# Performance work log

Hardware: AMD Instinct MI355X
Metric: run time of the kernel (lower is better)

The kernel has to match this reference:

```python
import jax, jax.numpy as jnp
import numpy as np

VOXEL_LENGTH = 1.2


def grid_sample_3d_border(vol, grid):
    """torch.nn.functional.grid_sample (5D, bilinear, align_corners=False,
    padding_mode='border') with grid flattened to (B, N, 3) in (x, y, z) order.
    vol: (B, C, D, H, W). Returns (B, C, N)."""

    def sample_one(v, g):
        C, D, H, W = v.shape
        x, y, z = g[:, 0], g[:, 1], g[:, 2]
        # align_corners=False unnormalization
        ix = ((x + 1.0) * W - 1.0) * 0.5
        iy = ((y + 1.0) * H - 1.0) * 0.5
        iz = ((z + 1.0) * D - 1.0) * 0.5
        ix0f, iy0f, iz0f = jnp.floor(ix), jnp.floor(iy), jnp.floor(iz)
        wx, wy, wz = ix - ix0f, iy - iy0f, iz - iz0f
        # border padding: clamp indices, keep unclamped weights
        x0 = jnp.clip(ix0f, 0, W - 1).astype(jnp.int32)
        x1 = jnp.clip(ix0f + 1, 0, W - 1).astype(jnp.int32)
        y0 = jnp.clip(iy0f, 0, H - 1).astype(jnp.int32)
        y1 = jnp.clip(iy0f + 1, 0, H - 1).astype(jnp.int32)
        z0 = jnp.clip(iz0f, 0, D - 1).astype(jnp.int32)
        z1 = jnp.clip(iz0f + 1, 0, D - 1).astype(jnp.int32)
        vflat = v.reshape(C, D * H * W)

        def gather(zi, yi, xi):  # -> (C, N)
            return vflat[:, (zi * H + yi) * W + xi]

        out = (
            gather(z0, y0, x0) * ((1 - wz) * (1 - wy) * (1 - wx))
            + gather(z0, y0, x1) * ((1 - wz) * (1 - wy) * wx)
            + gather(z0, y1, x0) * ((1 - wz) * wy * (1 - wx))
            + gather(z0, y1, x1) * ((1 - wz) * wy * wx)
            + gather(z1, y0, x0) * (wz * (1 - wy) * (1 - wx))
            + gather(z1, y0, x1) * (wz * (1 - wy) * wx)
            + gather(z1, y1, x0) * (wz * wy * (1 - wx))
            + gather(z1, y1, x1) * (wz * wy * wx)
        )
        return out

    return jax.vmap(sample_one)(vol, grid)


def setup_inputs() -> dict:
    key = jax.random.key(0)
    ks = jax.random.split(key, 16)
    B, IMG, STEPS = 2, 64, 24
    N = IMG * IMG * STEPS
    C_IN, HID, RES = 32, 256, 32
    # points in world space, inside the voxel cube [-0.6, 0.6]
    points = jax.random.uniform(ks[0], (B, N, 3), jnp.float32) * 1.2 - 0.6
    feature_volume = jax.random.normal(ks[1], (B, C_IN, RES, RES, RES), jnp.float32)

    def lin(k, fan_in, fan_out, scale):
        kw, kb = jax.random.split(k)
        W = jax.random.uniform(kw, (fan_out, fan_in), jnp.float32, -scale, scale)
        b = jax.random.uniform(kb, (fan_out,), jnp.float32, -scale, scale)
        return W, b

    freq = 12.0
    W0, b0 = lin(ks[2], C_IN, HID, 1.0 / C_IN)  # first_layer_film_sine_init
    W1, b1 = lin(ks[3], HID, HID, float(np.sqrt(6.0 / HID) / freq))
    W2, b2 = lin(ks[4], HID, HID, float(np.sqrt(6.0 / HID) / freq))
    W3, b3 = lin(ks[5], HID, HID, float(np.sqrt(6.0 / HID) / freq))
    Wf, bf = lin(ks[6], HID, 4, float(np.sqrt(6.0 / HID) / freq))
    return {
        "points": points, "feature_volume": feature_volume,
        "W0": W0, "b0": b0, "W1": W1, "b1": b1, "W2": W2, "b2": b2,
        "W3": W3, "b3": b3, "Wf": Wf, "bf": bf,
        "img_size": 64, "num_steps": 24,
    }


def reference(points, feature_volume, W0, b0, W1, b1, W2, b2, W3, b3, Wf, bf,
              img_size, num_steps):
    grid = points / (VOXEL_LENGTH / 2.0)  # (B, N, 3) in [-1, 1]
    feats = grid_sample_3d_border(feature_volume, grid)  # (B, C, N)
    x = feats.transpose(0, 2, 1)  # (B, N, C)
    for W, b in ((W0, b0), (W1, b1), (W2, b2), (W3, b3)):
        x = jnp.sin(jnp.einsum('bnc,hc->bnh', x, W) + b)
    rgb_sigma = jnp.einsum('bnh,oh->bno', x, Wf) + bf  # (B, N, 4)
    rgb = jax.nn.sigmoid(rgb_sigma[..., :3])
    sigma = rgb_sigma[..., 3:4]
    return jnp.concatenate([rgb, sigma], axis=-1)
```

## Files before the change

### kernel.cpp

```cpp
#include <hip/hip_runtime.h>
#include <math.h>

#define THREADS 256

typedef __attribute__((ext_vector_type(8))) short bf16x8;
typedef __attribute__((ext_vector_type(4))) float f32x4;

#define INV2PI 0.15915494309189535f

#define NCHUNK 26
#define STREAM_BYTES (NCHUNK * 16384)
#define SBIAS_BYTES 4096

__device__ __host__ __forceinline__ int sigma_k(int k) {
    return (k & 0xE1) | ((k & 0x04) << 2) | ((k & 0x18) >> 1) | (k & 0x02);
}

__device__ __forceinline__ ushort f2bf(float f) {
    union { float f; unsigned u; } v; v.f = f;
    unsigned r = v.u + 0x7FFFu + ((v.u >> 16) & 1u);
    return (ushort)(r >> 16);
}

__device__ __forceinline__ float fast_sigmoid(float x) {
    return 1.0f / (1.0f + __expf(-x));
}

__device__ __forceinline__ unsigned cvt_pk_bf16(float lo, float hi) {
    unsigned d;
    asm("v_cvt_pk_bf16_f32 %0, %1, %2" : "=v"(d) : "v"(lo), "v"(hi));
    return d;
}

__device__ __forceinline__ float hw_sin(float x) {
    float r;
    asm("v_sin_f32 %0, %1" : "=v"(r) : "v"(x));
    return r;
}

__global__ void build_frags(const float* __restrict__ W0,
                            const float* __restrict__ W1,
                            const float* __restrict__ W2,
                            const float* __restrict__ W3,
                            const float* __restrict__ Wf,
                            ushort* __restrict__ stream) {
    const int gid = blockIdx.x * 256 + threadIdx.x;
    const int f = gid >> 6;
    if (f >= 416) return;
    const int lane = gid & 63;
    const int p16 = lane & 15, g = lane >> 4;
    ushort* dst = stream + (size_t)f * 512 + lane * 8;

    if (f < 16) {
        const float* row = W0 + (size_t)(f * 16 + p16) * 32;
#pragma unroll
        for (int i = 0; i < 8; ++i) dst[i] = f2bf(row[8 * g + i] * INV2PI);
    } else if (f < 400) {
        const int t = f - 16;
        const int h = t >> 7;
        const int r = t & 127;
        const int sub = r >> 4;
        const int idx = r & 15;
        const int q = sub & 1;
        const int kq = sub >> 1;
        const int ksl = idx >> 3;
        const int ntl = idx & 7;
        const int nt = q * 8 + ntl;
        const int ks = kq * 2 + ksl;
        const float* W = (h == 0) ? W1 : (h == 1) ? W2 : W3;
        const float* row = W + (size_t)(nt * 16 + p16) * 256;
#pragma unroll
        for (int i = 0; i < 8; ++i) dst[i] = f2bf(row[sigma_k(32 * ks + 8 * g + i)] * INV2PI);
    } else if (f < 408) {
        const int ks = f - 400;
        if (p16 < 4) {
            const float* row = Wf + (size_t)p16 * 256;
#pragma unroll
            for (int i = 0; i < 8; ++i) dst[i] = f2bf(row[sigma_k(32 * ks + 8 * g + i)]);
        } else {
#pragma unroll
            for (int i = 0; i < 8; ++i) dst[i] = 0;
        }
    } else {
#pragma unroll
        for (int i = 0; i < 8; ++i) dst[i] = 0;
    }
}

__global__ void scale_biases(const float* __restrict__ b0, const float* __restrict__ b1,
                             const float* __restrict__ b2, const float* __restrict__ b3,
                             float* __restrict__ sb) {
    const int i = blockIdx.x * 256 + threadIdx.x;
    const int l = i >> 8, j = i & 255;
    const float* b = (l == 0) ? b0 : (l == 1) ? b1 : (l == 2) ? b2 : b3;
    sb[i] = b[j] * INV2PI;
}

__global__ void vol_chlast(const float* __restrict__ vol, float* __restrict__ dst, int nvox) {
    int v = blockIdx.x * 256 + threadIdx.x;
    if (v >= nvox) return;
    const int b = v >> 15, idx = v & 32767;
    const float* s = vol + (size_t)b * 32 * 32768 + idx;
    float* d = dst + (size_t)v * 32;
#pragma unroll
    for (int c = 0; c < 32; ++c) d[c] = s[(size_t)c * 32768];
}

#define MF(a, b, c) __builtin_amdgcn_mfma_f32_16x16x32_bf16((a), (b), (c), 0, 0, 0)

__global__ __launch_bounds__(THREADS, 2)
void siren_pl(const float* __restrict__ points,
              const float* __restrict__ vol,
              const float* __restrict__ bfin,
              const ushort* __restrict__ Wstream,
              const float* __restrict__ sb,
              const float* __restrict__ volcl, int use_cl,
              float* __restrict__ out, long long total, int N) {
    __shared__ ushort ring[3 * 8192];

    const int tid = (int)threadIdx.x;
    const int w = tid >> 6;
    const int lane = tid & 63;
    const int p16 = lane & 15;
    const int g = lane >> 4;

    const long long base = (long long)blockIdx.x * 128;

    auto stage = [&](int c) {
        if (c >= NCHUNK) return;
        const ushort* src = Wstream + (size_t)c * 8192;
        ushort* dstbase = ring + (c % 3) * 8192;
#pragma unroll
        for (int q = 0; q < 4; ++q) {
            const int off = (q * 4 + w) * 512;
            __builtin_amdgcn_global_load_lds(
                (const __attribute__((address_space(1))) unsigned int*)(src + off + lane * 8),
                (__attribute__((address_space(3))) unsigned int*)(dstbase + off),
                16, 0, 0);
        }
    };
    stage(0);
    stage(1);
    stage(2);

    bf16x8 af0[2];
    {
#pragma unroll
        for (int ptt = 0; ptt < 2; ++ptt) {
            const long long gidx = base + w * 32 + ptt * 16 + p16;
            const long long gp = gidx < total ? gidx : total - 1;
            const int bi = (int)(gp / N);
            const float* pp = points + gp * 3;
            const float sc = 1.0f / 0.6f;
            const float ix = (pp[0] * sc + 1.0f) * 16.0f - 0.5f;
            const float iy = (pp[1] * sc + 1.0f) * 16.0f - 0.5f;
            const float iz = (pp[2] * sc + 1.0f) * 16.0f - 0.5f;
            const float fx = floorf(ix), fy = floorf(iy), fz = floorf(iz);
            const float wx = ix - fx, wy = iy - fy, wz = iz - fz;
            const int x0 = (int)fminf(fmaxf(fx, 0.0f), 31.0f);
            const int x1 = (int)fminf(fmaxf(fx + 1.0f, 0.0f), 31.0f);
            const int y0 = (int)fminf(fmaxf(fy, 0.0f), 31.0f);
            const int y1 = (int)fminf(fmaxf(fy + 1.0f, 0.0f), 31.0f);
            const int z0 = (int)fminf(fmaxf(fz, 0.0f), 31.0f);
            const int z1 = (int)fminf(fmaxf(fz + 1.0f, 0.0f), 31.0f);
            const int i000 = (z0 * 32 + y0) * 32 + x0, i001 = (z0 * 32 + y0) * 32 + x1;
            const int i010 = (z0 * 32 + y1) * 32 + x0, i011 = (z0 * 32 + y1) * 32 + x1;
            const int i100 = (z1 * 32 + y0) * 32 + x0, i101 = (z1 * 32 + y0) * 32 + x1;
            const int i110 = (z1 * 32 + y1) * 32 + x0, i111 = (z1 * 32 + y1) * 32 + x1;
            const float omx = 1.0f - wx, omy = 1.0f - wy, omz = 1.0f - wz;
            const float w000 = omz * omy * omx, w001 = omz * omy * wx;
            const float w010 = omz * wy * omx,  w011 = omz * wy * wx;
            const float w100 = wz * omy * omx,  w101 = wz * omy * wx;
            const float w110 = wz * wy * omx,   w111 = wz * wy * wx;

            f32x4 a[2];
            if (use_cl) {
                const float* vb = volcl + (size_t)bi * 32768 * 32 + g * 8;
#pragma unroll
                for (int h = 0; h < 2; ++h) {
                    const float* vh = vb + h * 4;
                    a[h]  = w000 * *(const f32x4*)(vh + (size_t)i000 * 32);
                    a[h] += w001 * *(const f32x4*)(vh + (size_t)i001 * 32);
                    a[h] += w010 * *(const f32x4*)(vh + (size_t)i010 * 32);
                    a[h] += w011 * *(const f32x4*)(vh + (size_t)i011 * 32);
                    a[h] += w100 * *(const f32x4*)(vh + (size_t)i100 * 32);
                    a[h] += w101 * *(const f32x4*)(vh + (size_t)i101 * 32);
                    a[h] += w110 * *(const f32x4*)(vh + (size_t)i110 * 32);
                    a[h] += w111 * *(const f32x4*)(vh + (size_t)i111 * 32);
                }
            } else {
                const float* vb = vol + ((size_t)bi * 32 + (size_t)g * 8) * 32768;
#pragma unroll
                for (int c = 0; c < 8; ++c) {
                    const float* vc = vb + (size_t)c * 32768;
                    a[c >> 2][c & 3] =
                        vc[i000] * w000 + vc[i001] * w001 + vc[i010] * w010 + vc[i011] * w011 +
                        vc[i100] * w100 + vc[i101] * w101 + vc[i110] * w110 + vc[i111] * w111;
                }
            }
            union { bf16x8 v; unsigned u[4]; } pk;
            pk.u[0] = cvt_pk_bf16(a[0][0], a[0][1]);
            pk.u[1] = cvt_pk_bf16(a[0][2], a[0][3]);
            pk.u[2] = cvt_pk_bf16(a[1][0], a[1][1]);
            pk.u[3] = cvt_pk_bf16(a[1][2], a[1][3]);
            af0[ptt] = pk.v;
        }
    }

    f32x4 accA[2][8];
    f32x4 accB[2][8];
    bf16x8 bfr[2][8];
    bf16x8 wreg[8];

    auto frag_at = [&](int slot, int idx) -> bf16x8 {
        return *(const bf16x8*)&ring[slot * 8192 + idx * 512 + lane * 8];
    };
    auto init_half = [&](f32x4 (&A)[2][8], const float* __restrict__ b, int ntbase) {
#pragma unroll
        for (int m = 0; m < 8; ++m) {
            const f32x4 bv = *(const f32x4*)&b[(ntbase + m) * 16 + 4 * g];
            A[0][m] = bv; A[1][m] = bv;
        }
    };
    auto pack_half = [&](f32x4 (&A)[2][8], int ksbase) {
#pragma unroll
        for (int ptt = 0; ptt < 2; ++ptt)
#pragma unroll
            for (int ks2 = 0; ks2 < 4; ++ks2) {
                union { bf16x8 v; unsigned u[4]; } pk;
#pragma unroll
                for (int j = 0; j < 4; ++j) {
                    const int m = 2 * ks2 + (j >> 1);
                    const int r = 2 * (j & 1);
                    pk.u[j] = cvt_pk_bf16(hw_sin(A[ptt][m][r]), hw_sin(A[ptt][m][r + 1]));
                }
                bfr[ptt][ksbase + ks2] = pk.v;
            }
    };
    auto mfma_half = [&](int kq, int ksl, f32x4 (&A)[2][8], int nslot, int nbase) {
        const bf16x8 bA = bfr[0][kq * 2 + ksl];
        const bf16x8 bB = bfr[1][kq * 2 + ksl];
        __builtin_amdgcn_s_setprio(1);
#pragma unroll
        for (int ntl = 0; ntl < 8; ++ntl) {
            A[0][ntl] = MF(wreg[ntl], bA, A[0][ntl]);
            A[1][ntl] = MF(wreg[ntl], bB, A[1][ntl]);
            wreg[ntl] = frag_at(nslot, nbase + ntl);
        }
        __builtin_amdgcn_s_setprio(0);
    };

    init_half(accA, sb, 0);
    init_half(accB, sb, 8);
    __syncthreads();

#pragma unroll
    for (int i = 0; i < 8; ++i) wreg[i] = frag_at(0, i);

    __builtin_amdgcn_s_setprio(1);
#pragma unroll
    for (int ntl = 0; ntl < 8; ++ntl) {
        accA[0][ntl] = MF(wreg[ntl], af0[0], accA[0][ntl]);
        accA[1][ntl] = MF(wreg[ntl], af0[1], accA[1][ntl]);
        wreg[ntl] = frag_at(0, 8 + ntl);
    }
#pragma unroll
    for (int ntl = 0; ntl < 8; ++ntl) {
        accB[0][ntl] = MF(wreg[ntl], af0[0], accB[0][ntl]);
        accB[1][ntl] = MF(wreg[ntl], af0[1], accB[1][ntl]);
        wreg[ntl] = frag_at(1, ntl);
    }
    __builtin_amdgcn_s_setprio(0);
    __syncthreads(); stage(3);

#define LCH(k, ACC, KQ)                                                \
        mfma_half(KQ, 0, ACC, ((cbase) + (k)) % 3, 8);                 \
        mfma_half(KQ, 1, ACC, ((cbase) + (k) + 1) % 3, 0);             \
        __syncthreads(); stage((cbase) + (k) + 3);

#define LAYER(CB, SBL)                                                 \
    do {                                                               \
        const int cbase = (CB);                                        \
        pack_half(accA, 0); init_half(accA, (SBL), 0);                 \
        LCH(0, accA, 0)                                                \
        pack_half(accB, 4); init_half(accB, (SBL), 8);                 \
        LCH(1, accB, 0)                                                \
        LCH(2, accA, 1)                                                \
        LCH(3, accB, 1)                                                \
        LCH(4, accA, 2)                                                \
        LCH(5, accB, 2)                                                \
        LCH(6, accA, 3)                                                \
        LCH(7, accB, 3)                                                \
    } while (0)

    LAYER(1,  sb + 256);
    LAYER(9,  sb + 512);
    LAYER(17, sb + 768);

    pack_half(accA, 0);
    pack_half(accB, 4);
    {
        f32x4 fo[2] = {{0, 0, 0, 0}, {0, 0, 0, 0}};
#pragma unroll
        for (int ks = 0; ks < 8; ++ks) {
            fo[0] = MF(wreg[ks], bfr[0][ks], fo[0]);
            fo[1] = MF(wreg[ks], bfr[1][ks], fo[1]);
        }
        if (g == 0) {
#pragma unroll
            for (int ptt = 0; ptt < 2; ++ptt) {
                const long long oi = base + w * 32 + ptt * 16 + p16;
                if (oi < total) {
                    float4 o;
                    o.x = fast_sigmoid(fo[ptt][0] + bfin[0]);
                    o.y = fast_sigmoid(fo[ptt][1] + bfin[1]);
                    o.z = fast_sigmoid(fo[ptt][2] + bfin[2]);
                    o.w = fo[ptt][3] + bfin[3];
                    *(float4*)(out + oi * 4) = o;
                }
            }
        }
    }
}

extern "C" void kernel_launch(void* const* d_in, const int* in_sizes, int n_in,
                              void* d_out, int out_size, void* d_ws, size_t ws_size,
                              hipStream_t stream) {
    const float* points = (const float*)d_in[0];
    const float* vol    = (const float*)d_in[1];
    const float* W0 = (const float*)d_in[2];
    const float* b0 = (const float*)d_in[3];
    const float* W1 = (const float*)d_in[4];
    const float* b1 = (const float*)d_in[5];
    const float* W2 = (const float*)d_in[6];
    const float* b2 = (const float*)d_in[7];
    const float* W3 = (const float*)d_in[8];
    const float* b3 = (const float*)d_in[9];
    const float* Wf = (const float*)d_in[10];
    const float* bf = (const float*)d_in[11];

    const int B = in_sizes[1] / (32 * 32 * 32 * 32);
    const int N = in_sizes[0] / (3 * B);
    const long long total = (long long)B * N;
    const int tiles = (int)((total + 127) / 128);

    ushort* Wstream = (ushort*)d_ws;
    float* sb = (float*)((char*)d_ws + STREAM_BYTES);
    build_frags<<<104, 256, 0, stream>>>(W0, W1, W2, W3, Wf, Wstream);
    scale_biases<<<4, 256, 0, stream>>>(b0, b1, b2, b3, sb);

    const size_t fixed = (size_t)STREAM_BYTES + SBIAS_BYTES;
    const int use_cl = (ws_size >= fixed + (size_t)B * 32768 * 32 * 4) ? 1 : 0;
    float* volcl = (float*)((char*)d_ws + fixed);
    if (use_cl) {
        const int nvox = B * 32768;
        vol_chlast<<<(nvox + 255) / 256, 256, 0, stream>>>(vol, volcl, nvox);
    }

    siren_pl<<<tiles, THREADS, 0, stream>>>(
        points, vol, bf, Wstream, sb, volcl, use_cl,
        (float*)d_out, total, N);
}
```

Measured before the change: 102.6 us.

## Switch SIREN MLP from 16x16x32 to 32x32x16 bf16 MFMA tiles

Replaces the 16x16x32 bf16 MFMA tiling with 32x32x16 tiles throughout the MLP. Weight fragments are re-laid out to match, with a new k-permutation so that accumulator outputs pack directly into the next layer's B operand. The grid-sample stage now produces 32-point fragments per wave. The aim is to reach higher MFMA throughput and issue fewer instructions with fewer LDS fragment reads per FLOP. In exchange the layout changes substantially, the accumulators use more registers, and the final layer wastes compute on padded rows.

Measured after the change: 128.9 us. +25.7%, slower.

```diff
diff --git a/kernel.cpp b/kernel.cpp
--- a/kernel.cpp
+++ b/kernel.cpp
@@ -5,6 +5,7 @@
 
 typedef __attribute__((ext_vector_type(8))) short bf16x8;
 typedef __attribute__((ext_vector_type(4))) float f32x4;
+typedef __attribute__((ext_vector_type(16))) float f32x16;
 
 #define INV2PI 0.15915494309189535f
 
@@ -12,8 +13,8 @@
 #define STREAM_BYTES (NCHUNK * 16384)
 #define SBIAS_BYTES 4096
 
-__device__ __host__ __forceinline__ int sigma_k(int k) {
-    return (k & 0xE1) | ((k & 0x04) << 2) | ((k & 0x18) >> 1) | (k & 0x02);
+__device__ __host__ __forceinline__ int sigma32(int k) {
+    return (k & ~0xC) | ((k & 4) << 1) | ((k & 8) >> 1);
 }
 
 __device__ __forceinline__ ushort f2bf(float f) {
@@ -48,42 +49,41 @@
     const int f = gid >> 6;
     if (f >= 416) return;
     const int lane = gid & 63;
-    const int p16 = lane & 15, g = lane >> 4;
+    const int row = lane & 31;
+    const int h = lane >> 5;
     ushort* dst = stream + (size_t)f * 512 + lane * 8;
 
     if (f < 16) {
-        const float* row = W0 + (size_t)(f * 16 + p16) * 32;
-#pragma unroll
-        for (int i = 0; i < 8; ++i) dst[i] = f2bf(row[8 * g + i] * INV2PI);
+        const int t = f >> 3, n = f & 7;
+        const float* r0 = W0 + (size_t)(n * 32 + row) * 32;
+#pragma unroll
+        for (int i = 0; i < 8; ++i) dst[i] = f2bf(r0[t * 16 + 8 * h + i] * INV2PI);
     } else if (f < 400) {
-        const int t = f - 16;
-        const int h = t >> 7;
-        const int r = t & 127;
+        const int tt = f - 16;
+        const int hl = tt >> 7;
+        const int r = tt & 127;
         const int sub = r >> 4;
         const int idx = r & 15;
         const int q = sub & 1;
         const int kq = sub >> 1;
-        const int ksl = idx >> 3;
-        const int ntl = idx & 7;
-        const int nt = q * 8 + ntl;
-        const int ks = kq * 2 + ksl;
-        const float* W = (h == 0) ? W1 : (h == 1) ? W2 : W3;
-        const float* row = W + (size_t)(nt * 16 + p16) * 256;
-#pragma unroll
-        for (int i = 0; i < 8; ++i) dst[i] = f2bf(row[sigma_k(32 * ks + 8 * g + i)] * INV2PI);
-    } else if (f < 408) {
-        const int ks = f - 400;
-        if (p16 < 4) {
-            const float* row = Wf + (size_t)p16 * 256;
-#pragma unroll
-            for (int i = 0; i < 8; ++i) dst[i] = f2bf(row[sigma_k(32 * ks + 8 * g + i)]);
+        const int ksl = idx >> 3, tl = (idx >> 2) & 1, nl = idx & 3;
+        const int n = q * 4 + nl;
+        const int t = kq * 4 + ksl * 2 + tl;
+        const float* W = (hl == 0) ? W1 : (hl == 1) ? W2 : W3;
+        const float* r0 = W + (size_t)(n * 32 + row) * 256;
+#pragma unroll
+        for (int i = 0; i < 8; ++i)
+            dst[i] = f2bf(r0[sigma32(t * 16 + 8 * h + i)] * INV2PI);
+    } else {
+        const int t = f - 400;
+        if (row < 4) {
+            const float* r0 = Wf + (size_t)row * 256;
+#pragma unroll
+            for (int i = 0; i < 8; ++i) dst[i] = f2bf(r0[sigma32(t * 16 + 8 * h + i)]);
         } else {
 #pragma unroll
             for (int i = 0; i < 8; ++i) dst[i] = 0;
         }
-    } else {
-#pragma unroll
-        for (int i = 0; i < 8; ++i) dst[i] = 0;
     }
 }
 
@@ -106,7 +106,7 @@
     for (int c = 0; c < 32; ++c) d[c] = s[(size_t)c * 32768];
 }
 
-#define MF(a, b, c) __builtin_amdgcn_mfma_f32_16x16x32_bf16((a), (b), (c), 0, 0, 0)
+#define MF32(a, b, c) __builtin_amdgcn_mfma_f32_32x32x16_bf16((a), (b), (c), 0, 0, 0)
 
 __global__ __launch_bounds__(THREADS, 2)
 void siren_pl(const float* __restrict__ points,
@@ -121,8 +121,8 @@
     const int tid = (int)threadIdx.x;
     const int w = tid >> 6;
     const int lane = tid & 63;
-    const int p16 = lane & 15;
-    const int g = lane >> 4;
+    const int p32 = lane & 31;
+    const int h = lane >> 5;
 
     const long long base = (long long)blockIdx.x * 128;
 
@@ -145,113 +145,114 @@
 
     bf16x8 af0[2];
     {
-#pragma unroll
-        for (int ptt = 0; ptt < 2; ++ptt) {
-            const long long gidx = base + w * 32 + ptt * 16 + p16;
-            const long long gp = gidx < total ? gidx : total - 1;
-            const int bi = (int)(gp / N);
-            const float* pp = points + gp * 3;
-            const float sc = 1.0f / 0.6f;
-            const float ix = (pp[0] * sc + 1.0f) * 16.0f - 0.5f;
-            const float iy = (pp[1] * sc + 1.0f) * 16.0f - 0.5f;
-            const float iz = (pp[2] * sc + 1.0f) * 16.0f - 0.5f;
-            const float fx = floorf(ix), fy = floorf(iy), fz = floorf(iz);
-            const float wx = ix - fx, wy = iy - fy, wz = iz - fz;
-            const int x0 = (int)fminf(fmaxf(fx, 0.0f), 31.0f);
-            const int x1 = (int)fminf(fmaxf(fx + 1.0f, 0.0f), 31.0f);
-            const int y0 = (int)fminf(fmaxf(fy, 0.0f), 31.0f);
-            const int y1 = (int)fminf(fmaxf(fy + 1.0f, 0.0f), 31.0f);
-            const int z0 = (int)fminf(fmaxf(fz, 0.0f), 31.0f);
-            const int z1 = (int)fminf(fmaxf(fz + 1.0f, 0.0f), 31.0f);
-            const int i000 = (z0 * 32 + y0) * 32 + x0, i001 = (z0 * 32 + y0) * 32 + x1;
-            const int i010 = (z0 * 32 + y1) * 32 + x0, i011 = (z0 * 32 + y1) * 32 + x1;
-            const int i100 = (z1 * 32 + y0) * 32 + x0, i101 = (z1 * 32 + y0) * 32 + x1;
-            const int i110 = (z1 * 32 + y1) * 32 + x0, i111 = (z1 * 32 + y1) * 32 + x1;
-            const float omx = 1.0f - wx, omy = 1.0f - wy, omz = 1.0f - wz;
-            const float w000 = omz * omy * omx, w001 = omz * omy * wx;
-            const float w010 = omz * wy * omx,  w011 = omz * wy * wx;
-            const float w100 = wz * omy * omx,  w101 = wz * omy * wx;
-            const float w110 = wz * wy * omx,   w111 = wz * wy * wx;
-
-            f32x4 a[2];
-            if (use_cl) {
-                const float* vb = volcl + (size_t)bi * 32768 * 32 + g * 8;
-#pragma unroll
-                for (int h = 0; h < 2; ++h) {
-                    const float* vh = vb + h * 4;
-                    a[h]  = w000 * *(const f32x4*)(vh + (size_t)i000 * 32);
-                    a[h] += w001 * *(const f32x4*)(vh + (size_t)i001 * 32);
-                    a[h] += w010 * *(const f32x4*)(vh + (size_t)i010 * 32);
-                    a[h] += w011 * *(const f32x4*)(vh + (size_t)i011 * 32);
-                    a[h] += w100 * *(const f32x4*)(vh + (size_t)i100 * 32);
-                    a[h] += w101 * *(const f32x4*)(vh + (size_t)i101 * 32);
-                    a[h] += w110 * *(const f32x4*)(vh + (size_t)i110 * 32);
-                    a[h] += w111 * *(const f32x4*)(vh + (size_t)i111 * 32);
-                }
-            } else {
-                const float* vb = vol + ((size_t)bi * 32 + (size_t)g * 8) * 32768;
-#pragma unroll
-                for (int c = 0; c < 8; ++c) {
-                    const float* vc = vb + (size_t)c * 32768;
-                    a[c >> 2][c & 3] =
-                        vc[i000] * w000 + vc[i001] * w001 + vc[i010] * w010 + vc[i011] * w011 +
-                        vc[i100] * w100 + vc[i101] * w101 + vc[i110] * w110 + vc[i111] * w111;
-                }
-            }
+        const long long gidx = base + w * 32 + p32;
+        const long long gp = gidx < total ? gidx : total - 1;
+        const int bi = (int)(gp / N);
+        const float* pp = points + gp * 3;
+        const float sc = 1.0f / 0.6f;
+        const float ix = (pp[0] * sc + 1.0f) * 16.0f - 0.5f;
+        const float iy = (pp[1] * sc + 1.0f) * 16.0f - 0.5f;
+        const float iz = (pp[2] * sc + 1.0f) * 16.0f - 0.5f;
+        const float fx = floorf(ix), fy = floorf(iy), fz = floorf(iz);
+        const float wx = ix - fx, wy = iy - fy, wz = iz - fz;
+        const int x0 = (int)fminf(fmaxf(fx, 0.0f), 31.0f);
+        const int x1 = (int)fminf(fmaxf(fx + 1.0f, 0.0f), 31.0f);
+        const int y0 = (int)fminf(fmaxf(fy, 0.0f), 31.0f);
+        const int y1 = (int)fminf(fmaxf(fy + 1.0f, 0.0f), 31.0f);
+        const int z0 = (int)fminf(fmaxf(fz, 0.0f), 31.0f);
+        const int z1 = (int)fminf(fmaxf(fz + 1.0f, 0.0f), 31.0f);
+        const int i000 = (z0 * 32 + y0) * 32 + x0, i001 = (z0 * 32 + y0) * 32 + x1;
+        const int i010 = (z0 * 32 + y1) * 32 + x0, i011 = (z0 * 32 + y1) * 32 + x1;
+        const int i100 = (z1 * 32 + y0) * 32 + x0, i101 = (z1 * 32 + y0) * 32 + x1;
+        const int i110 = (z1 * 32 + y1) * 32 + x0, i111 = (z1 * 32 + y1) * 32 + x1;
+        const float omx = 1.0f - wx, omy = 1.0f - wy, omz = 1.0f - wz;
+        const float w000 = omz * omy * omx, w001 = omz * omy * wx;
+        const float w010 = omz * wy * omx,  w011 = omz * wy * wx;
+        const float w100 = wz * omy * omx,  w101 = wz * omy * wx;
+        const float w110 = wz * wy * omx,   w111 = wz * wy * wx;
+
+        f32x4 a[4];
+        if (use_cl) {
+            const float* vb = volcl + (size_t)bi * 32768 * 32;
+            const int co[4] = {8 * h, 8 * h + 4, 16 + 8 * h, 16 + 8 * h + 4};
+#pragma unroll
+            for (int s = 0; s < 4; ++s) {
+                const float* vh = vb + co[s];
+                a[s]  = w000 * *(const f32x4*)(vh + (size_t)i000 * 32);
+                a[s] += w001 * *(const f32x4*)(vh + (size_t)i001 * 32);
+                a[s] += w010 * *(const f32x4*)(vh + (size_t)i010 * 32);
+                a[s] += w011 * *(const f32x4*)(vh + (size_t)i011 * 32);
+                a[s] += w100 * *(const f32x4*)(vh + (size_t)i100 * 32);
+                a[s] += w101 * *(const f32x4*)(vh + (size_t)i101 * 32);
+                a[s] += w110 * *(const f32x4*)(vh + (size_t)i110 * 32);
+                a[s] += w111 * *(const f32x4*)(vh + (size_t)i111 * 32);
+            }
+        } else {
+            const float* vb = vol + (size_t)bi * 32 * 32768;
+#pragma unroll
+            for (int c = 0; c < 16; ++c) {
+                const int ch = (c < 8) ? (8 * h + c) : (16 + 8 * h + (c - 8));
+                const float* vc = vb + (size_t)ch * 32768;
+                a[c >> 2][c & 3] =
+                    vc[i000] * w000 + vc[i001] * w001 + vc[i010] * w010 + vc[i011] * w011 +
+                    vc[i100] * w100 + vc[i101] * w101 + vc[i110] * w110 + vc[i111] * w111;
+            }
+        }
+#pragma unroll
+        for (int t = 0; t < 2; ++t) {
             union { bf16x8 v; unsigned u[4]; } pk;
-            pk.u[0] = cvt_pk_bf16(a[0][0], a[0][1]);
-            pk.u[1] = cvt_pk_bf16(a[0][2], a[0][3]);
-            pk.u[2] = cvt_pk_bf16(a[1][0], a[1][1]);
-            pk.u[3] = cvt_pk_bf16(a[1][2], a[1][3]);
-            af0[ptt] = pk.v;
-        }
-    }
-
-    f32x4 accA[2][8];
-    f32x4 accB[2][8];
-    bf16x8 bfr[2][8];
+            pk.u[0] = cvt_pk_bf16(a[2 * t][0], a[2 * t][1]);
+            pk.u[1] = cvt_pk_bf16(a[2 * t][2], a[2 * t][3]);
+            pk.u[2] = cvt_pk_bf16(a[2 * t + 1][0], a[2 * t + 1][1]);
+            pk.u[3] = cvt_pk_bf16(a[2 * t + 1][2], a[2 * t + 1][3]);
+            af0[t] = pk.v;
+        }
+    }
+
+    f32x16 accA[4];
+    f32x16 accB[4];
+    bf16x8 bfr[16];
     bf16x8 wreg[8];
 
     auto frag_at = [&](int slot, int idx) -> bf16x8 {
         return *(const bf16x8*)&ring[slot * 8192 + idx * 512 + lane * 8];
     };
-    auto init_half = [&](f32x4 (&A)[2][8], const float* __restrict__ b, int ntbase) {
-#pragma unroll
-        for (int m = 0; m < 8; ++m) {
-            const f32x4 bv = *(const f32x4*)&b[(ntbase + m) * 16 + 4 * g];
-            A[0][m] = bv; A[1][m] = bv;
-        }
-    };
-    auto pack_half = [&](f32x4 (&A)[2][8], int ksbase) {
-#pragma unroll
-        for (int ptt = 0; ptt < 2; ++ptt)
-#pragma unroll
-            for (int ks2 = 0; ks2 < 4; ++ks2) {
+    auto init_half = [&](f32x16 (&A)[4], const float* __restrict__ b, int ngbase) {
+#pragma unroll
+        for (int n = 0; n < 4; ++n)
+#pragma unroll
+            for (int v = 0; v < 4; ++v) {
+                const f32x4 bv = *(const f32x4*)&b[(ngbase + n) * 32 + 8 * v + 4 * h];
+#pragma unroll
+                for (int e = 0; e < 4; ++e) A[n][4 * v + e] = bv[e];
+            }
+    };
+    auto pack_half = [&](f32x16 (&A)[4], int tb) {
+#pragma unroll
+        for (int n = 0; n < 4; ++n)
+#pragma unroll
+            for (int tt = 0; tt < 2; ++tt) {
                 union { bf16x8 v; unsigned u[4]; } pk;
 #pragma unroll
-                for (int j = 0; j < 4; ++j) {
-                    const int m = 2 * ks2 + (j >> 1);
-                    const int r = 2 * (j & 1);
-                    pk.u[j] = cvt_pk_bf16(hw_sin(A[ptt][m][r]), hw_sin(A[ptt][m][r + 1]));
-                }
-                bfr[ptt][ksbase + ks2] = pk.v;
-            }
-    };
-    auto mfma_half = [&](int kq, int ksl, f32x4 (&A)[2][8], int nslot, int nbase) {
-        const bf16x8 bA = bfr[0][kq * 2 + ksl];
-        const bf16x8 bB = bfr[1][kq * 2 + ksl];
+                for (int j = 0; j < 4; ++j)
+                    pk.u[j] = cvt_pk_bf16(hw_sin(A[n][tt * 8 + 2 * j]),
+                                          hw_sin(A[n][tt * 8 + 2 * j + 1]));
+                bfr[tb + 2 * n + tt] = pk.v;
+            }
+    };
+    auto mfma_half = [&](int kq, int ksl, f32x16 (&A)[4], int nslot, int nbase) {
         __builtin_amdgcn_s_setprio(1);
 #pragma unroll
-        for (int ntl = 0; ntl < 8; ++ntl) {
-            A[0][ntl] = MF(wreg[ntl], bA, A[0][ntl]);
-            A[1][ntl] = MF(wreg[ntl], bB, A[1][ntl]);
-            wreg[ntl] = frag_at(nslot, nbase + ntl);
+        for (int idx = 0; idx < 8; ++idx) {
+            const int tl = idx >> 2, nl = idx & 3;
+            A[nl] = MF32(wreg[idx], bfr[kq * 4 + ksl * 2 + tl], A[nl]);
+            wreg[idx] = frag_at(nslot, nbase + idx);
         }
         __builtin_amdgcn_s_setprio(0);
     };
 
     init_half(accA, sb, 0);
-    init_half(accB, sb, 8);
+    init_half(accB, sb, 4);
     __syncthreads();
 
 #pragma unroll
@@ -259,65 +260,67 @@
 
     __builtin_amdgcn_s_setprio(1);
 #pragma unroll
-    for (int ntl = 0; ntl < 8; ++ntl) {
-        accA[0][ntl] = MF(wreg[ntl], af0[0], accA[0][ntl]);
-        accA[1][ntl] = MF(wreg[ntl], af0[1], accA[1][ntl]);
-        wreg[ntl] = frag_at(0, 8 + ntl);
-    }
-#pragma unroll
-    for (int ntl = 0; ntl < 8; ++ntl) {
-        accB[0][ntl] = MF(wreg[ntl], af0[0], accB[0][ntl]);
-        accB[1][ntl] = MF(wreg[ntl], af0[1], accB[1][ntl]);
-        wreg[ntl] = frag_at(1, ntl);
+    for (int n = 0; n < 8; ++n) {
+        if (n < 4) accA[n] = MF32(wreg[n], af0[0], accA[n]);
+        else       accB[n - 4] = MF32(wreg[n], af0[0], accB[n - 4]);
+        wreg[n] = frag_at(0, 8 + n);
+    }
+#pragma unroll
+    for (int n = 0; n < 8; ++n) {
+        if (n < 4) accA[n] = MF32(wreg[n], af0[1], accA[n]);
+        else       accB[n - 4] = MF32(wreg[n], af0[1], accB[n - 4]);
+        wreg[n] = frag_at(1, n);
     }
     __builtin_amdgcn_s_setprio(0);
     __syncthreads(); stage(3);
 
-#define LCH(k, ACC, KQ)                                                \
-        mfma_half(KQ, 0, ACC, ((cbase) + (k)) % 3, 8);                 \
-        mfma_half(KQ, 1, ACC, ((cbase) + (k) + 1) % 3, 0);             \
-        __syncthreads(); stage((cbase) + (k) + 3);
-
-#define LAYER(CB, SBL)                                                 \
+#define LCH(CK, KQ, ACC)                                               \
+        mfma_half(KQ, 0, ACC, (CK) % 3, 8);                            \
+        mfma_half(KQ, 1, ACC, ((CK) + 1) % 3, 0);                      \
+        __syncthreads(); stage((CK) + 3);
+
+#define LAYER(CB, SBL, NG)                                             \
     do {                                                               \
-        const int cbase = (CB);                                        \
         pack_half(accA, 0); init_half(accA, (SBL), 0);                 \
-        LCH(0, accA, 0)                                                \
-        pack_half(accB, 4); init_half(accB, (SBL), 8);                 \
-        LCH(1, accB, 0)                                                \
-        LCH(2, accA, 1)                                                \
-        LCH(3, accB, 1)                                                \
-        LCH(4, accA, 2)                                                \
-        LCH(5, accB, 2)                                                \
-        LCH(6, accA, 3)                                                \
-        LCH(7, accB, 3)                                                \
+        LCH((CB) + 0, 0, accA)                                         \
+        pack_half(accB, 8); init_half(accB, (SBL), 4);                 \
+        LCH((CB) + 1, 0, accB)                                         \
+        LCH((CB) + 2, 1, accA)                                         \
+        LCH((CB) + 3, 1, accB)                                         \
+        LCH((CB) + 4, 2, accA)                                         \
+        LCH((CB) + 5, 2, accB)                                         \
+        LCH((CB) + 6, 3, accA)                                         \
+        LCH((CB) + 7, 3, accB)                                         \
     } while (0)
 
-    LAYER(1,  sb + 256);
-    LAYER(9,  sb + 512);
-    LAYER(17, sb + 768);
+    LAYER(1,  sb + 256, 0);
+    LAYER(9,  sb + 512, 0);
+    LAYER(17, sb + 768, 0);
 
     pack_half(accA, 0);
-    pack_half(accB, 4);
+    pack_half(accB, 8);
     {
-        f32x4 fo[2] = {{0, 0, 0, 0}, {0, 0, 0, 0}};
-#pragma unroll
-        for (int ks = 0; ks < 8; ++ks) {
-            fo[0] = MF(wreg[ks], bfr[0][ks], fo[0]);
-            fo[1] = MF(wreg[ks], bfr[1][ks], fo[1]);
-        }
-        if (g == 0) {
-#pragma unroll
-            for (int ptt = 0; ptt < 2; ++ptt) {
-                const long long oi = base + w * 32 + ptt * 16 + p16;
-                if (oi < total) {
-                    float4 o;
-                    o.x = fast_sigmoid(fo[ptt][0] + bfin[0]);
-                    o.y = fast_sigmoid(fo[ptt][1] + bfin[1]);
-                    o.z = fast_sigmoid(fo[ptt][2] + bfin[2]);
-                    o.w = fo[ptt][3] + bfin[3];
-                    *(float4*)(out + oi * 4) = o;
-                }
+        f32x16 fo = {};
+        __builtin_amdgcn_s_setprio(1);
+#pragma unroll
+        for (int t = 0; t < 8; ++t) {
+            fo = MF32(wreg[t], bfr[t], fo);
+            wreg[t] = frag_at(25 % 3, 8 + t);
+        }
+#pragma unroll
+        for (int t = 0; t < 8; ++t)
+            fo = MF32(wreg[t], bfr[8 + t], fo);
+        __builtin_amdgcn_s_setprio(0);
+
+        if (h == 0) {
+            const long long oi = base + w * 32 + p32;
+            if (oi < total) {
+                float4 o;
+                o.x = fast_sigmoid(fo[0] + bfin[0]);
+                o.y = fast_sigmoid(fo[1] + bfin[1]);
+                o.z = fast_sigmoid(fo[2] + bfin[2]);
+                o.w = fo[3] + bfin[3];
+                *(float4*)(out + oi * 4) = o;
             }
         }
     }
```

## Load second half of each weight chunk directly from L2, halve LDS ring

Applied to the files above, without the earlier changes.

Each 16 KB weight chunk is now split in two. Only the first half is staged into the LDS ring through global_load_lds. The second half is read by each lane straight from global memory (L2) into registers during the MFMA loop. This halves LDS footprint and staging traffic, which could allow more occupancy and fewer async copies. The cost is global-load latency on the critical MFMA path, since the loaded fragments feed the very next MFMA batch.

After: 119.5 us. 1.16x slower.

```diff
diff --git a/kernel.cpp b/kernel.cpp
--- a/kernel.cpp
+++ b/kernel.cpp
@@ -116,7 +116,7 @@
               const float* __restrict__ sb,
               const float* __restrict__ volcl, int use_cl,
               float* __restrict__ out, long long total, int N) {
-    __shared__ ushort ring[3 * 8192];
+    __shared__ ushort ring[3 * 4096];
 
     const int tid = (int)threadIdx.x;
     const int w = tid >> 6;
@@ -126,12 +126,14 @@
 
     const long long base = (long long)blockIdx.x * 128;
 
+    const ushort* __restrict__ l2p = Wstream + lane * 8;
+
     auto stage = [&](int c) {
         if (c >= NCHUNK) return;
         const ushort* src = Wstream + (size_t)c * 8192;
-        ushort* dstbase = ring + (c % 3) * 8192;
-#pragma unroll
-        for (int q = 0; q < 4; ++q) {
+        ushort* dstbase = ring + (c % 3) * 4096;
+#pragma unroll
+        for (int q = 0; q < 2; ++q) {
             const int off = (q * 4 + w) * 512;
             __builtin_amdgcn_global_load_lds(
                 (const __attribute__((address_space(1))) unsigned int*)(src + off + lane * 8),
@@ -213,7 +215,10 @@
     bf16x8 wreg[8];
 
     auto frag_at = [&](int slot, int idx) -> bf16x8 {
-        return *(const bf16x8*)&ring[slot * 8192 + idx * 512 + lane * 8];
+        return *(const bf16x8*)&ring[slot * 4096 + idx * 512 + lane * 8];
+    };
+    auto l2_frag = [&](int c, int idx) -> bf16x8 {
+        return *(const bf16x8*)(l2p + (size_t)c * 8192 + idx * 512);
     };
     auto init_half = [&](f32x4 (&A)[2][8], const float* __restrict__ b, int ntbase) {
 #pragma unroll
@@ -237,15 +242,27 @@
                 bfr[ptt][ksbase + ks2] = pk.v;
             }
     };
-    auto mfma_half = [&](int kq, int ksl, f32x4 (&A)[2][8], int nslot, int nbase) {
-        const bf16x8 bA = bfr[0][kq * 2 + ksl];
-        const bf16x8 bB = bfr[1][kq * 2 + ksl];
+    auto mfma_half_l2 = [&](int kq, f32x4 (&A)[2][8], int c) {
+        const bf16x8 bA = bfr[0][kq * 2];
+        const bf16x8 bB = bfr[1][kq * 2];
         __builtin_amdgcn_s_setprio(1);
 #pragma unroll
         for (int ntl = 0; ntl < 8; ++ntl) {
             A[0][ntl] = MF(wreg[ntl], bA, A[0][ntl]);
             A[1][ntl] = MF(wreg[ntl], bB, A[1][ntl]);
-            wreg[ntl] = frag_at(nslot, nbase + ntl);
+            wreg[ntl] = l2_frag(c, 8 + ntl);
+        }
+        __builtin_amdgcn_s_setprio(0);
+    };
+    auto mfma_half_lds = [&](int kq, f32x4 (&A)[2][8], int nslot) {
+        const bf16x8 bA = bfr[0][kq * 2 + 1];
+        const bf16x8 bB = bfr[1][kq * 2 + 1];
+        __builtin_amdgcn_s_setprio(1);
+#pragma unroll
+        for (int ntl = 0; ntl < 8; ++ntl) {
+            A[0][ntl] = MF(wreg[ntl], bA, A[0][ntl]);
+            A[1][ntl] = MF(wreg[ntl], bB, A[1][ntl]);
+            wreg[ntl] = frag_at(nslot, ntl);
         }
         __builtin_amdgcn_s_setprio(0);
     };
@@ -262,7 +279,7 @@
     for (int ntl = 0; ntl < 8; ++ntl) {
         accA[0][ntl] = MF(wreg[ntl], af0[0], accA[0][ntl]);
         accA[1][ntl] = MF(wreg[ntl], af0[1], accA[1][ntl]);
-        wreg[ntl] = frag_at(0, 8 + ntl);
+        wreg[ntl] = l2_frag(0, 8 + ntl);
     }
 #pragma unroll
     for (int ntl = 0; ntl < 8; ++ntl) {
@@ -273,24 +290,23 @@
     __builtin_amdgcn_s_setprio(0);
     __syncthreads(); stage(3);
 
-#define LCH(k, ACC, KQ)                                                \
-        mfma_half(KQ, 0, ACC, ((cbase) + (k)) % 3, 8);                 \
-        mfma_half(KQ, 1, ACC, ((cbase) + (k) + 1) % 3, 0);             \
-        __syncthreads(); stage((cbase) + (k) + 3);
+#define LCH(CK, KQ, ACC)                                               \
+        mfma_half_l2(KQ, ACC, CK);                                     \
+        mfma_half_lds(KQ, ACC, ((CK) + 1) % 3);                        \
+        __syncthreads(); stage((CK) + 3);
 
 #define LAYER(CB, SBL)                                                 \
     do {                                                               \
-        const int cbase = (CB);                                        \
         pack_half(accA, 0); init_half(accA, (SBL), 0);                 \
-        LCH(0, accA, 0)                                                \
+        LCH((CB) + 0, 0, accA)                                         \
         pack_half(accB, 4); init_half(accB, (SBL), 8);                 \
-        LCH(1, accB, 0)                                                \
-        LCH(2, accA, 1)                                                \
-        LCH(3, accB, 1)                                                \
-        LCH(4, accA, 2)                                                \
-        LCH(5, accB, 2)                                                \
-        LCH(6, accA, 3)                                                \
-        LCH(7, accB, 3)                                                \
+        LCH((CB) + 1, 0, accB)                                         \
+        LCH((CB) + 2, 1, accA)                                         \
+        LCH((CB) + 3, 1, accB)                                         \
+        LCH((CB) + 4, 2, accA)                                         \
+        LCH((CB) + 5, 2, accB)                                         \
+        LCH((CB) + 6, 3, accA)                                         \
+        LCH((CB) + 7, 3, accB)                                         \
     } while (0)
 
     LAYER(1,  sb + 256);
```

## Switch SIREN MLP matmuls from bf16 to fp8 MFMA with scaled weights

Applied to the files above, without the earlier changes.

Weights and activations are now quantised to fp8 (e4m3) instead of bf16 and multiplied with the fp8 16x16x32 MFMA. Weights and biases are pre-scaled by 512 to keep them in fp8 range, and accumulators are rescaled by 1/512 before sin and the final output. This halves the weight stream bytes and LDS ring traffic and uses the higher-throughput fp8 matrix path. In exchange, fp8 precision through four sine layers may push the output error past tolerance.

New measurement: 101.1 us. No clear change (-1.4%).

```diff
diff --git a/kernel.cpp b/kernel.cpp
--- a/kernel.cpp
+++ b/kernel.cpp
@@ -3,39 +3,40 @@
 
 #define THREADS 256
 
-typedef __attribute__((ext_vector_type(8))) short bf16x8;
 typedef __attribute__((ext_vector_type(4))) float f32x4;
 
 #define INV2PI 0.15915494309189535f
+#define WS     512.0f
+#define INV_WS 0.001953125f
 
 #define NCHUNK 26
-#define STREAM_BYTES (NCHUNK * 16384)
+#define STREAM_BYTES (NCHUNK * 8192)
 #define SBIAS_BYTES 4096
 
 __device__ __host__ __forceinline__ int sigma_k(int k) {
     return (k & 0xE1) | ((k & 0x04) << 2) | ((k & 0x18) >> 1) | (k & 0x02);
 }
 
-__device__ __forceinline__ ushort f2bf(float f) {
-    union { float f; unsigned u; } v; v.f = f;
-    unsigned r = v.u + 0x7FFFu + ((v.u >> 16) & 1u);
-    return (ushort)(r >> 16);
-}
-
 __device__ __forceinline__ float fast_sigmoid(float x) {
     return 1.0f / (1.0f + __expf(-x));
-}
-
-__device__ __forceinline__ unsigned cvt_pk_bf16(float lo, float hi) {
-    unsigned d;
-    asm("v_cvt_pk_bf16_f32 %0, %1, %2" : "=v"(d) : "v"(lo), "v"(hi));
-    return d;
 }
 
 __device__ __forceinline__ float hw_sin(float x) {
     float r;
     asm("v_sin_f32 %0, %1" : "=v"(r) : "v"(x));
     return r;
+}
+
+__device__ __forceinline__ unsigned pk8_lo(float a, float b) {
+    return (unsigned)__builtin_amdgcn_cvt_pk_fp8_f32(a, b, 0, false);
+}
+__device__ __forceinline__ unsigned pk8_hi(unsigned old, float a, float b) {
+    return (unsigned)__builtin_amdgcn_cvt_pk_fp8_f32(a, b, (int)old, true);
+}
+__device__ __forceinline__ long long pk8x8(const float v[8]) {
+    const unsigned u0 = pk8_hi(pk8_lo(v[0], v[1]), v[2], v[3]);
+    const unsigned u1 = pk8_hi(pk8_lo(v[4], v[5]), v[6], v[7]);
+    return (long long)(((unsigned long long)u1 << 32) | u0);
 }
 
 __global__ void build_frags(const float* __restrict__ W0,
@@ -43,18 +44,19 @@
                             const float* __restrict__ W2,
                             const float* __restrict__ W3,
                             const float* __restrict__ Wf,
-                            ushort* __restrict__ stream) {
+                            unsigned char* __restrict__ stream) {
     const int gid = blockIdx.x * 256 + threadIdx.x;
     const int f = gid >> 6;
     if (f >= 416) return;
     const int lane = gid & 63;
     const int p16 = lane & 15, g = lane >> 4;
-    ushort* dst = stream + (size_t)f * 512 + lane * 8;
-
+    unsigned char* dst = stream + (size_t)f * 512 + lane * 8;
+
+    float v[8];
     if (f < 16) {
         const float* row = W0 + (size_t)(f * 16 + p16) * 32;
 #pragma unroll
-        for (int i = 0; i < 8; ++i) dst[i] = f2bf(row[8 * g + i] * INV2PI);
+        for (int i = 0; i < 8; ++i) v[i] = row[8 * g + i] * (INV2PI * WS);
     } else if (f < 400) {
         const int t = f - 16;
         const int h = t >> 7;
@@ -70,21 +72,24 @@
         const float* W = (h == 0) ? W1 : (h == 1) ? W2 : W3;
         const float* row = W + (size_t)(nt * 16 + p16) * 256;
 #pragma unroll
-        for (int i = 0; i < 8; ++i) dst[i] = f2bf(row[sigma_k(32 * ks + 8 * g + i)] * INV2PI);
+        for (int i = 0; i < 8; ++i)
+            v[i] = row[sigma_k(32 * ks + 8 * g + i)] * (INV2PI * WS);
     } else if (f < 408) {
         const int ks = f - 400;
         if (p16 < 4) {
             const float* row = Wf + (size_t)p16 * 256;
 #pragma unroll
-            for (int i = 0; i < 8; ++i) dst[i] = f2bf(row[sigma_k(32 * ks + 8 * g + i)]);
+            for (int i = 0; i < 8; ++i) v[i] = row[sigma_k(32 * ks + 8 * g + i)] * WS;
         } else {
 #pragma unroll
-            for (int i = 0; i < 8; ++i) dst[i] = 0;
+            for (int i = 0; i < 8; ++i) v[i] = 0.0f;
         }
     } else {
 #pragma unroll
-        for (int i = 0; i < 8; ++i) dst[i] = 0;
-    }
+        for (int i = 0; i < 8; ++i) v[i] = 0.0f;
+    }
+    const long long pk = pk8x8(v);
+    *(long long*)dst = pk;
 }
 
 __global__ void scale_biases(const float* __restrict__ b0, const float* __restrict__ b1,
@@ -93,7 +98,7 @@
     const int i = blockIdx.x * 256 + threadIdx.x;
     const int l = i >> 8, j = i & 255;
     const float* b = (l == 0) ? b0 : (l == 1) ? b1 : (l == 2) ? b2 : b3;
-    sb[i] = b[j] * INV2PI;
+    sb[i] = b[j] * (INV2PI * WS);
 }
 
 __global__ void vol_chlast(const float* __restrict__ vol, float* __restrict__ dst, int nvox) {
@@ -106,17 +111,17 @@
     for (int c = 0; c < 32; ++c) d[c] = s[(size_t)c * 32768];
 }
 
-#define MF(a, b, c) __builtin_amdgcn_mfma_f32_16x16x32_bf16((a), (b), (c), 0, 0, 0)
+#define MF8(a, b, c) __builtin_amdgcn_mfma_f32_16x16x32_fp8_fp8((a), (b), (c), 0, 0, 0)
 
 __global__ __launch_bounds__(THREADS, 2)
 void siren_pl(const float* __restrict__ points,
               const float* __restrict__ vol,
               const float* __restrict__ bfin,
-              const ushort* __restrict__ Wstream,
+              const unsigned char* __restrict__ Wstream,
               const float* __restrict__ sb,
               const float* __restrict__ volcl, int use_cl,
               float* __restrict__ out, long long total, int N) {
-    __shared__ ushort ring[3 * 8192];
+    __shared__ __align__(16) unsigned char ring[3 * 8192];
 
     const int tid = (int)threadIdx.x;
     const int w = tid >> 6;
@@ -128,13 +133,13 @@
 
     auto stage = [&](int c) {
         if (c >= NCHUNK) return;
-        const ushort* src = Wstream + (size_t)c * 8192;
-        ushort* dstbase = ring + (c % 3) * 8192;
-#pragma unroll
-        for (int q = 0; q < 4; ++q) {
-            const int off = (q * 4 + w) * 512;
+        const unsigned char* src = Wstream + (size_t)c * 8192;
+        unsigned char* dstbase = ring + (c % 3) * 8192;
+#pragma unroll
+        for (int q = 0; q < 2; ++q) {
+            const int off = (q * 4 + w) * 1024;
             __builtin_amdgcn_global_load_lds(
-                (const __attribute__((address_space(1))) unsigned int*)(src + off + lane * 8),
+                (const __attribute__((address_space(1))) unsigned int*)(src + off + lane * 16),
                 (__attribute__((address_space(3))) unsigned int*)(dstbase + off),
                 16, 0, 0);
         }
@@ -143,7 +148,7 @@
     stage(1);
     stage(2);
 
-    bf16x8 af0[2];
+    long long af0[2];
     {
 #pragma unroll
         for (int ptt = 0; ptt < 2; ++ptt) {
@@ -198,22 +203,19 @@
                         vc[i100] * w100 + vc[i101] * w101 + vc[i110] * w110 + vc[i111] * w111;
                 }
             }
-            union { bf16x8 v; unsigned u[4]; } pk;
-            pk.u[0] = cvt_pk_bf16(a[0][0], a[0][1]);
-            pk.u[1] = cvt_pk_bf16(a[0][2], a[0][3]);
-            pk.u[2] = cvt_pk_bf16(a[1][0], a[1][1]);
-            pk.u[3] = cvt_pk_bf16(a[1][2], a[1][3]);
-            af0[ptt] = pk.v;
+            const unsigned u0 = pk8_hi(pk8_lo(a[0][0], a[0][1]), a[0][2], a[0][3]);
+            const unsigned u1 = pk8_hi(pk8_lo(a[1][0], a[1][1]), a[1][2], a[1][3]);
+            af0[ptt] = (long long)(((unsigned long long)u1 << 32) | u0);
         }
     }
 
     f32x4 accA[2][8];
     f32x4 accB[2][8];
-    bf16x8 bfr[2][8];
-    bf16x8 wreg[8];
-
-    auto frag_at = [&](int slot, int idx) -> bf16x8 {
-        return *(const bf16x8*)&ring[slot * 8192 + idx * 512 + lane * 8];
+    long long bfr[2][8];
+    long long wreg[8];
+
+    auto frag_at = [&](int slot, int idx) -> long long {
+        return *(const long long*)&ring[slot * 8192 + idx * 512 + lane * 8];
     };
     auto init_half = [&](f32x4 (&A)[2][8], const float* __restrict__ b, int ntbase) {
 #pragma unroll
@@ -227,24 +229,24 @@
         for (int ptt = 0; ptt < 2; ++ptt)
 #pragma unroll
             for (int ks2 = 0; ks2 < 4; ++ks2) {
-                union { bf16x8 v; unsigned u[4]; } pk;
-#pragma unroll
-                for (int j = 0; j < 4; ++j) {
-                    const int m = 2 * ks2 + (j >> 1);
-                    const int r = 2 * (j & 1);
-                    pk.u[j] = cvt_pk_bf16(hw_sin(A[ptt][m][r]), hw_sin(A[ptt][m][r + 1]));
+                const int m0 = 2 * ks2, m1 = 2 * ks2 + 1;
+                float s[8];
+#pragma unroll
+                for (int r = 0; r < 4; ++r) {
+                    s[r]     = hw_sin(A[ptt][m0][r] * INV_WS);
+                    s[4 + r] = hw_sin(A[ptt][m1][r] * INV_WS);
                 }
-                bfr[ptt][ksbase + ks2] = pk.v;
+                bfr[ptt][ksbase + ks2] = pk8x8(s);
             }
     };
     auto mfma_half = [&](int kq, int ksl, f32x4 (&A)[2][8], int nslot, int nbase) {
-        const bf16x8 bA = bfr[0][kq * 2 + ksl];
-        const bf16x8 bB = bfr[1][kq * 2 + ksl];
+        const long long bA = bfr[0][kq * 2 + ksl];
+        const long long bB = bfr[1][kq * 2 + ksl];
         __builtin_amdgcn_s_setprio(1);
 #pragma unroll
         for (int ntl = 0; ntl < 8; ++ntl) {
-            A[0][ntl] = MF(wreg[ntl], bA, A[0][ntl]);
-            A[1][ntl] = MF(wreg[ntl], bB, A[1][ntl]);
+            A[0][ntl] = MF8(wreg[ntl], bA, A[0][ntl]);
+            A[1][ntl] = MF8(wreg[ntl], bB, A[1][ntl]);
             wreg[ntl] = frag_at(nslot, nbase + ntl);
         }
         __builtin_amdgcn_s_setprio(0);
@@ -260,14 +262,14 @@
     __builtin_amdgcn_s_setprio(1);
 #pragma unroll
     for (int ntl = 0; ntl < 8; ++ntl) {
-        accA[0][ntl] = MF(wreg[ntl], af0[0], accA[0][ntl]);
-        accA[1][ntl] = MF(wreg[ntl], af0[1], accA[1][ntl]);
+        accA[0][ntl] = MF8(wreg[ntl], af0[0], accA[0][ntl]);
+        accA[1][ntl] = MF8(wreg[ntl], af0[1], accA[1][ntl]);
         wreg[ntl] = frag_at(0, 8 + ntl);
     }
 #pragma unroll
     for (int ntl = 0; ntl < 8; ++ntl) {
-        accB[0][ntl] = MF(wreg[ntl], af0[0], accB[0][ntl]);
-        accB[1][ntl] = MF(wreg[ntl], af0[1], accB[1][ntl]);
+        accB[0][ntl] = MF8(wreg[ntl], af0[0], accB[0][ntl]);
+        accB[1][ntl] = MF8(wreg[ntl], af0[1], accB[1][ntl]);
         wreg[ntl] = frag_at(1, ntl);
     }
     __builtin_amdgcn_s_setprio(0);
@@ -303,8 +305,8 @@
         f32x4 fo[2] = {{0, 0, 0, 0}, {0, 0, 0, 0}};
 #pragma unroll
         for (int ks = 0; ks < 8; ++ks) {
-            fo[0] = MF(wreg[ks], bfr[0][ks], fo[0]);
-            fo[1] = MF(wreg[ks], bfr[1][ks], fo[1]);
+            fo[0] = MF8(wreg[ks], bfr[0][ks], fo[0]);
+            fo[1] = MF8(wreg[ks], bfr[1][ks], fo[1]);
         }
         if (g == 0) {
 #pragma unroll
@@ -312,10 +314,10 @@
                 const long long oi = base + w * 32 + ptt * 16 + p16;
                 if (oi < total) {
                     float4 o;
-                    o.x = fast_sigmoid(fo[ptt][0] + bfin[0]);
-                    o.y = fast_sigmoid(fo[ptt][1] + bfin[1]);
-                    o.z = fast_sigmoid(fo[ptt][2] + bfin[2]);
-                    o.w = fo[ptt][3] + bfin[3];
+                    o.x = fast_sigmoid(fo[ptt][0] * INV_WS + bfin[0]);
+                    o.y = fast_sigmoid(fo[ptt][1] * INV_WS + bfin[1]);
+                    o.z = fast_sigmoid(fo[ptt][2] * INV_WS + bfin[2]);
+                    o.w = fo[ptt][3] * INV_WS + bfin[3];
                     *(float4*)(out + oi * 4) = o;
                 }
             }
@@ -344,7 +346,7 @@
     const long long total = (long long)B * N;
     const int tiles = (int)((total + 127) / 128);
 
-    ushort* Wstream = (ushort*)d_ws;
+    unsigned char* Wstream = (unsigned char*)d_ws;
     float* sb = (float*)((char*)d_ws + STREAM_BYTES);
     build_frags<<<104, 256, 0, stream>>>(W0, W1, W2, W3, Wf, Wstream);
     scale_biases<<<4, 256, 0, stream>>>(b0, b1, b2, b3, sb);
```
